# Optimization experiments

Measured on AMD Instinct MI355X. Metric: run time of the kernel, lower is better.

## Reference

```python
import jax, jax.numpy as jnp
import numpy as np

N = 100000   # nodes
E = 1600000  # edges
IN = 768     # in_dim
H = 128      # hidden_dim
G = 64       # graphs per batch


def setup_inputs() -> dict:
    key = jax.random.key(0)
    ks = jax.random.split(key, 9)
    x = jax.random.normal(ks[0], (N, IN), jnp.float32)
    edge_index = jax.random.randint(ks[1], (2, E), 0, N, dtype=jnp.int64)
    batch = jnp.sort(jax.random.randint(ks[2], (N,), 0, G, dtype=jnp.int64))
    W1 = jax.random.normal(ks[3], (IN, H), jnp.float32) / np.float32(np.sqrt(IN))
    b1 = jax.random.normal(ks[4], (H,), jnp.float32) * 0.01
    W2 = jax.random.normal(ks[5], (H, H), jnp.float32) / np.float32(np.sqrt(H))
    b2 = jax.random.normal(ks[6], (H,), jnp.float32) * 0.01
    Wh = jax.random.normal(ks[7], (H, 2), jnp.float32) / np.float32(np.sqrt(H))
    bh = jax.random.normal(ks[8], (2,), jnp.float32) * 0.01
    return dict(x=x, edge_index=edge_index, batch=batch, W1=W1, b1=b1,
                W2=W2, b2=b2, Wh=Wh, bh=bh, num_graphs=G)


def gcn_conv(x, src, dst, W, b, n):
    # PyG GCNConv default: add self-loops (already in src/dst), symmetric norm.
    deg = jax.ops.segment_sum(jnp.ones_like(dst, x.dtype), dst, num_segments=n)
    dis = jnp.where(deg > 0, jax.lax.rsqrt(deg), jnp.zeros_like(deg))
    h = x @ W                                   # [n, out]
    norm = (dis[src] * dis[dst])[:, None]       # [E+n, 1]
    out = jax.ops.segment_sum(h[src] * norm, dst, num_segments=n)
    return out + b


def reference(x, edge_index, batch, W1, b1, W2, b2, Wh, bh, num_graphs):
    n = x.shape[0]
    loop = jnp.arange(n, dtype=edge_index.dtype)
    src = jnp.concatenate([edge_index[0], loop])
    dst = jnp.concatenate([edge_index[1], loop])
    h = jax.nn.relu(gcn_conv(x, src, dst, W1, b1, n))   # dropout = eval identity
    h = jax.nn.relu(gcn_conv(h, src, dst, W2, b2, n))
    summed = jax.ops.segment_sum(h, batch, num_segments=num_graphs)
    counts = jax.ops.segment_sum(jnp.ones((n, 1), h.dtype), batch, num_segments=num_graphs)
    emb = summed / jnp.maximum(counts, 1.0)             # global_mean_pool
    return emb @ Wh + bh
```

## Files before the change

### kernel.cpp

```cpp
#include <hip/hip_runtime.h>
#include <hip/hip_bf16.h>
#include <hip/hip_fp16.h>

static constexpr int N_NODES  = 100000;
static constexpr int N_EDGES  = 1600000;
static constexpr int DIM_IN   = 768;
static constexpr int DIM_H    = 128;
static constexpr int N_GRAPHS = 64;
static constexpr int NB_SCAN  = (N_NODES + 255) / 256;

typedef __attribute__((ext_vector_type(8))) _Float16 half8;
typedef __attribute__((ext_vector_type(4))) float f32x4;

__global__ void k_convW(const float* __restrict__ W1, const float* __restrict__ W2,
                        _Float16* __restrict__ W1t, _Float16* __restrict__ W2t) {
    int i = blockIdx.x * 256 + threadIdx.x;
    const int total1 = DIM_IN * DIM_H;
    if (i < total1) {
        int k = i >> 7, n = i & 127;
        W1t[(size_t)n * DIM_IN + k] = (_Float16)W1[i];
    } else if (i < total1 + DIM_H * DIM_H) {
        int j = i - total1;
        int k = j >> 7, n = j & 127;
        W2t[(size_t)n * DIM_H + k] = (_Float16)W2[j];
    }
}

__global__ void k_scan1(const int* __restrict__ indeg, int* __restrict__ rp,
                        int* __restrict__ bsum, float* __restrict__ dis) {
    __shared__ int s[256];
    int t = threadIdx.x;
    int i = blockIdx.x * 256 + t;
    int v = (i < N_NODES) ? indeg[i] : 0;
    s[t] = v;
    __syncthreads();
    for (int off = 1; off < 256; off <<= 1) {
        int x = (t >= off) ? s[t - off] : 0;
        __syncthreads();
        s[t] += x;
        __syncthreads();
    }
    if (i < N_NODES) {
        rp[i] = s[t] - v;
        dis[i] = rsqrtf((float)v + 1.0f);
    }
    if (t == 255) bsum[blockIdx.x] = s[255];
}

__global__ void k_scan2(int* __restrict__ bsum, const int* __restrict__ batch,
                        int* __restrict__ gstart) {
    __shared__ int s[512];
    int t = threadIdx.x;
    int v = (t < NB_SCAN) ? bsum[t] : 0;
    s[t] = v;
    __syncthreads();
    for (int off = 1; off < 512; off <<= 1) {
        int x = (t >= off) ? s[t - off] : 0;
        __syncthreads();
        s[t] += x;
        __syncthreads();
    }
    if (t < NB_SCAN) bsum[t] = s[t] - v;
    if (t <= N_GRAPHS) {
        int lo = 0, hi = N_NODES;
        while (lo < hi) {
            int mid = (lo + hi) >> 1;
            if (batch[mid] < t) lo = mid + 1; else hi = mid;
        }
        gstart[t] = lo;
    }
}

__global__ void k_fixup(const int* __restrict__ rp, const int* __restrict__ bsum,
                        int* __restrict__ rpg, int* __restrict__ cursor2) {
    int i = blockIdx.x * 256 + threadIdx.x;
    if (i < N_NODES) {
        int v = rp[i] + bsum[i >> 8];
        rpg[i] = v;
        cursor2[i] = v;
    }
}

__global__ void k_scatter(const int* __restrict__ esrc, const int* __restrict__ edst,
                          const float* __restrict__ dis,
                          int* __restrict__ cursor2, uint2* __restrict__ csrw) {
    int e = blockIdx.x * 256 + threadIdx.x;
    if (e >= N_EDGES) return;
    int d = edst[e];
    int sv = esrc[e];
    int pos = atomicAdd(&cursor2[d], 1);
    uint2 val;
    val.x = (uint)sv;
    val.y = __float_as_uint(dis[sv]);
    csrw[pos] = val;
}

#define BKV 64
#define LDSTR 72

template<int K, bool AFP32, bool FUSE_INDEG>
__global__ __launch_bounds__(256) void k_gemm_mfma(const void* __restrict__ Av,
                                                   const _Float16* __restrict__ Wt,
                                                   _Float16* __restrict__ C,
                                                   int nrows,
                                                   const int* __restrict__ edst,
                                                   int* __restrict__ indeg,
                                                   int gemm_blocks) {
    __shared__ ushort As[64 * LDSTR];
    __shared__ ushort Bs[128 * LDSTR];

    if (FUSE_INDEG && (int)blockIdx.x >= gemm_blocks) {
        int e = (blockIdx.x - gemm_blocks) * 256 + threadIdx.x;
        if (e < N_EDGES) atomicAdd(&indeg[edst[e]], 1);
        return;
    }

    const int t = threadIdx.x;
    const int row0 = blockIdx.x * 64;
    const int sa_row = t >> 2;
    const int sa_col = (t & 3) * 16;
    const int sw_row = t >> 1;
    const int sw_col = (t & 1) * 32;
    const int l = t & 63;
    const int wv = t >> 6;
    const int wm = wv >> 1, wn = wv & 1;
    const int lr = l & 15;
    const int lk8 = (l >> 4) * 8;
    const bool arow_ok = (row0 + sa_row < nrows);

    f32x4 acc[2][4];
    const f32x4 zero = {0.f, 0.f, 0.f, 0.f};
    #pragma unroll
    for (int m = 0; m < 2; ++m)
        #pragma unroll
        for (int n = 0; n < 4; ++n) acc[m][n] = zero;

    for (int k0 = 0; k0 < K; k0 += BKV) {
        if (AFP32) {
            union { _Float16 h[16]; uint4 q[2]; } cv;
            float f[16];
            if (arow_ok) {
                const float4* Ap = (const float4*)((const float*)Av +
                    (size_t)(row0 + sa_row) * K + k0 + sa_col);
                #pragma unroll
                for (int i = 0; i < 4; ++i) *(float4*)&f[4 * i] = Ap[i];
            } else {
                #pragma unroll
                for (int i = 0; i < 16; ++i) f[i] = 0.f;
            }
            #pragma unroll
            for (int i = 0; i < 16; ++i) cv.h[i] = (_Float16)f[i];
            *(uint4*)&As[sa_row * LDSTR + sa_col]     = cv.q[0];
            *(uint4*)&As[sa_row * LDSTR + sa_col + 8] = cv.q[1];
        } else {
            uint4 q0 = {0, 0, 0, 0}, q1 = {0, 0, 0, 0};
            if (arow_ok) {
                const uint4* Ap = (const uint4*)((const _Float16*)Av +
                    (size_t)(row0 + sa_row) * K + k0 + sa_col);
                q0 = Ap[0]; q1 = Ap[1];
            }
            *(uint4*)&As[sa_row * LDSTR + sa_col]     = q0;
            *(uint4*)&As[sa_row * LDSTR + sa_col + 8] = q1;
        }
        {
            const uint4* Wp = (const uint4*)(Wt + (size_t)sw_row * K + k0 + sw_col);
            uint4 w0 = Wp[0], w1 = Wp[1], w2 = Wp[2], w3 = Wp[3];
            *(uint4*)&Bs[sw_row * LDSTR + sw_col + 0]  = w0;
            *(uint4*)&Bs[sw_row * LDSTR + sw_col + 8]  = w1;
            *(uint4*)&Bs[sw_row * LDSTR + sw_col + 16] = w2;
            *(uint4*)&Bs[sw_row * LDSTR + sw_col + 24] = w3;
        }
        __syncthreads();

        #pragma unroll
        for (int ks2 = 0; ks2 < 2; ++ks2) {
            half8 a[2], b[4];
            #pragma unroll
            for (int m = 0; m < 2; ++m)
                a[m] = *(const half8*)&As[(wm * 32 + m * 16 + lr) * LDSTR + ks2 * 32 + lk8];
            #pragma unroll
            for (int n = 0; n < 4; ++n)
                b[n] = *(const half8*)&Bs[(wn * 64 + n * 16 + lr) * LDSTR + ks2 * 32 + lk8];
            #pragma unroll
            for (int m = 0; m < 2; ++m)
                #pragma unroll
                for (int n = 0; n < 4; ++n)
                    acc[m][n] = __builtin_amdgcn_mfma_f32_16x16x32_f16(a[m], b[n], acc[m][n], 0, 0, 0);
        }
        __syncthreads();
    }

    #pragma unroll
    for (int m = 0; m < 2; ++m) {
        #pragma unroll
        for (int n = 0; n < 4; ++n) {
            int col = wn * 64 + n * 16 + lr;
            #pragma unroll
            for (int j = 0; j < 4; ++j) {
                int row = row0 + wm * 32 + m * 16 + (l >> 4) * 4 + j;
                if (row < nrows)
                    C[(size_t)row * DIM_H + col] = (_Float16)acc[m][n][j];
            }
        }
    }
}

__device__ __forceinline__ void acc8(uint4 u, float w, float* a) {
    __half2 h0 = *(__half2*)&u.x;
    __half2 h1 = *(__half2*)&u.y;
    __half2 h2 = *(__half2*)&u.z;
    __half2 h3 = *(__half2*)&u.w;
    a[0] += __low2float(h0) * w; a[1] += __high2float(h0) * w;
    a[2] += __low2float(h1) * w; a[3] += __high2float(h1) * w;
    a[4] += __low2float(h2) * w; a[5] += __high2float(h2) * w;
    a[6] += __low2float(h3) * w; a[7] += __high2float(h3) * w;
}

__global__ __launch_bounds__(256) void k_agg(const _Float16* __restrict__ hin,
                                             const uint2* __restrict__ csrw,
                                             const int* __restrict__ rpg,
                                             const int* __restrict__ indeg,
                                             const float* __restrict__ dis,
                                             const float* __restrict__ bias,
                                             _Float16* __restrict__ hout) {
    int node = (blockIdx.x * 256 + threadIdx.x) >> 6;
    int lane = threadIdx.x & 63;
    if (node >= N_NODES) return;
    int q  = lane >> 4;
    int cl = lane & 15;
    float di = dis[node];
    int beg = rpg[node];
    int cnt = indeg[node];

    float a[8] = {0.f, 0.f, 0.f, 0.f, 0.f, 0.f, 0.f, 0.f};

    {
        uint s; float w;
        if (q == 0)             { s = (uint)node; w = di * di; }
        else if (q - 1 < cnt)   { uint2 p = csrw[beg + q - 1]; s = p.x; w = __uint_as_float(p.y) * di; }
        else                    { s = (uint)node; w = 0.f; }
        uint4 u = ((const uint4*)(hin + (size_t)s * DIM_H))[cl];
        acc8(u, w, a);
    }
    const uint2* cp = csrw + beg + 3;
    int m = cnt - 3;
    int i = 0;
    for (; i + 8 <= m; i += 8) {
        uint2 p0 = cp[i + q];
        uint2 p1 = cp[i + 4 + q];
        float w0 = __uint_as_float(p0.y) * di;
        float w1 = __uint_as_float(p1.y) * di;
        uint4 u0 = ((const uint4*)(hin + (size_t)p0.x * DIM_H))[cl];
        uint4 u1 = ((const uint4*)(hin + (size_t)p1.x * DIM_H))[cl];
        acc8(u0, w0, a);
        acc8(u1, w1, a);
    }
    for (; i < m; i += 4) {
        int idx = i + q;
        uint s; float w;
        if (idx < m) { uint2 p = cp[idx]; s = p.x; w = __uint_as_float(p.y) * di; }
        else         { s = (uint)node;    w = 0.f; }
        uint4 u = ((const uint4*)(hin + (size_t)s * DIM_H))[cl];
        acc8(u, w, a);
    }

    #pragma unroll
    for (int j = 0; j < 8; ++j) {
        a[j] += __shfl_xor(a[j], 16);
        a[j] += __shfl_xor(a[j], 32);
    }

    if (q == 0) {
        float4 b0 = ((const float4*)bias)[cl * 2];
        float4 b1 = ((const float4*)bias)[cl * 2 + 1];
        __half2 h0 = __floats2half2_rn(fmaxf(a[0] + b0.x, 0.f), fmaxf(a[1] + b0.y, 0.f));
        __half2 h1 = __floats2half2_rn(fmaxf(a[2] + b0.z, 0.f), fmaxf(a[3] + b0.w, 0.f));
        __half2 h2 = __floats2half2_rn(fmaxf(a[4] + b1.x, 0.f), fmaxf(a[5] + b1.y, 0.f));
        __half2 h3 = __floats2half2_rn(fmaxf(a[6] + b1.z, 0.f), fmaxf(a[7] + b1.w, 0.f));
        uint4 o;
        o.x = *(uint*)&h0; o.y = *(uint*)&h1; o.z = *(uint*)&h2; o.w = *(uint*)&h3;
        ((uint4*)(hout + (size_t)node * DIM_H))[cl] = o;
    }
}

#define PSPLIT 8
__global__ __launch_bounds__(256) void k_pool(const _Float16* __restrict__ h,
                                              const int* __restrict__ gstart,
                                              float* __restrict__ pooled2) {
    int g  = blockIdx.x >> 3;
    int sp = blockIdx.x & 7;
    int r0 = gstart[g], r1 = gstart[g + 1];
    int count = r1 - r0;
    int chunk = (count + PSPLIT - 1) / PSPLIT;
    int aS = r0 + sp * chunk;
    int bE = min(aS + chunk, r1);
    int c  = threadIdx.x & 63;
    int rr = threadIdx.x >> 6;
    float s0a = 0.f, s1a = 0.f, s0b = 0.f, s1b = 0.f;
    int r = aS + rr;
    for (; r + 4 < bE; r += 8) {
        uint ua = ((const uint*)(h + (size_t)r * DIM_H))[c];
        uint ub = ((const uint*)(h + (size_t)(r + 4) * DIM_H))[c];
        __half2 ha = *(__half2*)&ua;
        __half2 hb = *(__half2*)&ub;
        s0a += __low2float(ha); s1a += __high2float(ha);
        s0b += __low2float(hb); s1b += __high2float(hb);
    }
    if (r < bE) {
        uint ua = ((const uint*)(h + (size_t)r * DIM_H))[c];
        __half2 ha = *(__half2*)&ua;
        s0a += __low2float(ha); s1a += __high2float(ha);
    }
    float s0 = s0a + s0b, s1 = s1a + s1b;
    __shared__ float sm0[4][64], sm1[4][64];
    sm0[rr][c] = s0; sm1[rr][c] = s1;
    __syncthreads();
    if (rr == 0) {
        float v0 = sm0[0][c] + sm0[1][c] + sm0[2][c] + sm0[3][c];
        float v1 = sm1[0][c] + sm1[1][c] + sm1[2][c] + sm1[3][c];
        float* dst = pooled2 + (size_t)(g * PSPLIT + sp) * DIM_H;
        dst[2 * c]     = v0;
        dst[2 * c + 1] = v1;
    }
}

__global__ __launch_bounds__(128) void k_head(const float* __restrict__ pooled2,
                                              const int* __restrict__ gstart,
                                              const float* __restrict__ Wh,
                                              const float* __restrict__ bh,
                                              float* __restrict__ out) {
    int g = blockIdx.x;
    int c = threadIdx.x;
    float s = 0.f;
    #pragma unroll
    for (int sp = 0; sp < PSPLIT; ++sp)
        s += pooled2[(size_t)(g * PSPLIT + sp) * DIM_H + c];
    float cntg = (float)(gstart[g + 1] - gstart[g]);
    float e = s / fmaxf(cntg, 1.0f);
    __shared__ float s0[128], s1[128];
    s0[c] = e * Wh[c * 2 + 0];
    s1[c] = e * Wh[c * 2 + 1];
    __syncthreads();
    for (int off = 64; off > 0; off >>= 1) {
        if (c < off) { s0[c] += s0[c + off]; s1[c] += s1[c + off]; }
        __syncthreads();
    }
    if (c == 0) {
        out[g * 2 + 0] = s0[0] + bh[0];
        out[g * 2 + 1] = s1[0] + bh[1];
    }
}

extern "C" void kernel_launch(void* const* d_in, const int* in_sizes, int n_in,
                              void* d_out, int out_size, void* d_ws, size_t ws_size,
                              hipStream_t stream) {
    const float* x    = (const float*)d_in[0];
    const int*   esrc = (const int*)d_in[1];
    const int*   edst = esrc + N_EDGES;
    const int*   batch= (const int*)d_in[2];
    const float* W1   = (const float*)d_in[3];
    const float* b1   = (const float*)d_in[4];
    const float* W2   = (const float*)d_in[5];
    const float* b2   = (const float*)d_in[6];
    const float* Wh   = (const float*)d_in[7];
    const float* bh   = (const float*)d_in[8];
    float* out = (float*)d_out;

    char* ws = (char*)d_ws;
    size_t off = 0;
    auto alloc = [&](size_t bytes) {
        void* p = ws + off;
        off += (bytes + 255) & ~(size_t)255;
        return p;
    };
    _Float16* bufZ   = (_Float16*)alloc((size_t)N_NODES * DIM_H * 2);
    _Float16* bufH   = (_Float16*)alloc((size_t)N_NODES * DIM_H * 2);
    float*    dis    = (float*)alloc((size_t)N_NODES * 4);
    int*      indeg  = (int*)  alloc((size_t)N_NODES * 4);
    int*      rp     = (int*)  alloc((size_t)N_NODES * 4);
    int*      rpg    = (int*)  alloc((size_t)N_NODES * 4);
    int*      cursor2= (int*)  alloc((size_t)N_NODES * 4);
    uint2*    csrw   = (uint2*)alloc((size_t)N_EDGES * 8);
    int*      bsum   = (int*)  alloc(512 * 4);
    float*    pooled2= (float*)alloc((size_t)N_GRAPHS * PSPLIT * DIM_H * 4);
    int*      gstart = (int*)  alloc((N_GRAPHS + 1) * 4);
    _Float16* W1t    = (_Float16*)alloc((size_t)DIM_IN * DIM_H * 2);
    _Float16* W2t    = (_Float16*)alloc((size_t)DIM_H * DIM_H * 2);

    hipMemsetAsync(indeg, 0, (size_t)N_NODES * 4, stream);

    int convblocks = (DIM_IN * DIM_H + DIM_H * DIM_H + 255) / 256;
    k_convW  <<<convblocks, 256, 0, stream>>>(W1, W2, W1t, W2t);

    int gblocks = (N_NODES + 63) / 64;
    int eblocks = (N_EDGES + 255) / 256;
    k_gemm_mfma<DIM_IN, true, true><<<gblocks + eblocks, 256, 0, stream>>>(
        x, W1t, bufZ, N_NODES, edst, indeg, gblocks);
    k_scan1  <<<NB_SCAN, 256, 0, stream>>>(indeg, rp, bsum, dis);
    k_scan2  <<<1, 512, 0, stream>>>(bsum, batch, gstart);
    k_fixup  <<<NB_SCAN, 256, 0, stream>>>(rp, bsum, rpg, cursor2);
    k_scatter<<<eblocks, 256, 0, stream>>>(esrc, edst, dis, cursor2, csrw);

    k_agg<<<(N_NODES + 3) / 4, 256, 0, stream>>>(bufZ, csrw, rpg, indeg, dis, b1, bufH);
    k_gemm_mfma<DIM_H, false, false><<<gblocks, 256, 0, stream>>>(
        bufH, W2t, bufZ, N_NODES, nullptr, nullptr, gblocks);
    k_agg<<<(N_NODES + 3) / 4, 256, 0, stream>>>(bufZ, csrw, rpg, indeg, dis, b2, bufH);

    k_pool<<<N_GRAPHS * PSPLIT, 256, 0, stream>>>(bufH, gstart, pooled2);
    k_head<<<N_GRAPHS, 128, 0, stream>>>(pooled2, gstart, Wh, bh, out);
}
```

Baseline: 386.6 us.

## Fold symmetric GCN normalization into row scaling and shrink CSR to source indices

Factors the per-edge weight dis[src]*dis[dst] out of aggregation. Source rows are pre-scaled by dis (the layer-1 features in a separate pass fused into the scatter launch, the layer-2 input by scaling the layer-1 aggregation output), and the destination factor is applied once per node. The CSR entry shrinks from 8 to 4 bytes, which halves edge-list traffic in both aggregations and drops the dis gather in the scatter. The cost is an extra read-modify-write pass over the layer-1 features and slightly different fp16 rounding.

New measurement: 425.0 us. +9.9%, slower.

```diff
diff --git a/kernel.cpp b/kernel.cpp
--- a/kernel.cpp
+++ b/kernel.cpp
@@ -81,18 +81,34 @@
     }
 }
 
-__global__ void k_scatter(const int* __restrict__ esrc, const int* __restrict__ edst,
-                          const float* __restrict__ dis,
-                          int* __restrict__ cursor2, uint2* __restrict__ csrw) {
-    int e = blockIdx.x * 256 + threadIdx.x;
-    if (e >= N_EDGES) return;
-    int d = edst[e];
-    int sv = esrc[e];
-    int pos = atomicAdd(&cursor2[d], 1);
-    uint2 val;
-    val.x = (uint)sv;
-    val.y = __float_as_uint(dis[sv]);
-    csrw[pos] = val;
+#define SCALE_U4 (N_NODES * DIM_H / 8)
+__global__ void k_scatscale(const int* __restrict__ esrc, const int* __restrict__ edst,
+                            int* __restrict__ cursor2, uint* __restrict__ csr,
+                            const float* __restrict__ dis, uint4* __restrict__ bufZ4,
+                            int scat_blocks) {
+    int b = blockIdx.x;
+    if (b < scat_blocks) {
+        int e = b * 256 + threadIdx.x;
+        if (e < N_EDGES) {
+            int d = edst[e];
+            int pos = atomicAdd(&cursor2[d], 1);
+            csr[pos] = (uint)esrc[e];
+        }
+        return;
+    }
+    int i = (b - scat_blocks) * 256 + threadIdx.x;
+    if (i >= SCALE_U4) return;
+    int row = i >> 4;
+    float d = dis[row];
+    uint4 u = bufZ4[i];
+    uint* w = (uint*)&u;
+    #pragma unroll
+    for (int j = 0; j < 4; ++j) {
+        __half2 h = *(__half2*)&w[j];
+        __half2 r = __floats2half2_rn(__low2float(h) * d, __high2float(h) * d);
+        w[j] = *(uint*)&r;
+    }
+    bufZ4[i] = u;
 }
 
 #define BKV 64
@@ -216,8 +232,9 @@
     a[6] += __low2float(h3) * w; a[7] += __high2float(h3) * w;
 }
 
+template<bool SCALE_OUT>
 __global__ __launch_bounds__(256) void k_agg(const _Float16* __restrict__ hin,
-                                             const uint2* __restrict__ csrw,
+                                             const uint* __restrict__ csr,
                                              const int* __restrict__ rpg,
                                              const int* __restrict__ indeg,
                                              const float* __restrict__ dis,
@@ -235,31 +252,29 @@
     float a[8] = {0.f, 0.f, 0.f, 0.f, 0.f, 0.f, 0.f, 0.f};
 
     {
-        uint s; float w;
-        if (q == 0)             { s = (uint)node; w = di * di; }
-        else if (q - 1 < cnt)   { uint2 p = csrw[beg + q - 1]; s = p.x; w = __uint_as_float(p.y) * di; }
+        uint s; float w = 1.f;
+        if (q == 0)             { s = (uint)node; }
+        else if (q - 1 < cnt)   { s = csr[beg + q - 1]; }
         else                    { s = (uint)node; w = 0.f; }
         uint4 u = ((const uint4*)(hin + (size_t)s * DIM_H))[cl];
         acc8(u, w, a);
     }
-    const uint2* cp = csrw + beg + 3;
+    const uint* cp = csr + beg + 3;
     int m = cnt - 3;
     int i = 0;
     for (; i + 8 <= m; i += 8) {
-        uint2 p0 = cp[i + q];
-        uint2 p1 = cp[i + 4 + q];
-        float w0 = __uint_as_float(p0.y) * di;
-        float w1 = __uint_as_float(p1.y) * di;
-        uint4 u0 = ((const uint4*)(hin + (size_t)p0.x * DIM_H))[cl];
-        uint4 u1 = ((const uint4*)(hin + (size_t)p1.x * DIM_H))[cl];
-        acc8(u0, w0, a);
-        acc8(u1, w1, a);
+        uint s0 = cp[i + q];
+        uint s1 = cp[i + 4 + q];
+        uint4 u0 = ((const uint4*)(hin + (size_t)s0 * DIM_H))[cl];
+        uint4 u1 = ((const uint4*)(hin + (size_t)s1 * DIM_H))[cl];
+        acc8(u0, 1.f, a);
+        acc8(u1, 1.f, a);
     }
     for (; i < m; i += 4) {
         int idx = i + q;
-        uint s; float w;
-        if (idx < m) { uint2 p = cp[idx]; s = p.x; w = __uint_as_float(p.y) * di; }
-        else         { s = (uint)node;    w = 0.f; }
+        uint s; float w = 1.f;
+        if (idx < m) { s = cp[idx]; }
+        else         { s = (uint)node; w = 0.f; }
         uint4 u = ((const uint4*)(hin + (size_t)s * DIM_H))[cl];
         acc8(u, w, a);
     }
@@ -273,13 +288,20 @@
     if (q == 0) {
         float4 b0 = ((const float4*)bias)[cl * 2];
         float4 b1 = ((const float4*)bias)[cl * 2 + 1];
-        __half2 h0 = __floats2half2_rn(fmaxf(a[0] + b0.x, 0.f), fmaxf(a[1] + b0.y, 0.f));
-        __half2 h1 = __floats2half2_rn(fmaxf(a[2] + b0.z, 0.f), fmaxf(a[3] + b0.w, 0.f));
-        __half2 h2 = __floats2half2_rn(fmaxf(a[4] + b1.x, 0.f), fmaxf(a[5] + b1.y, 0.f));
-        __half2 h3 = __floats2half2_rn(fmaxf(a[6] + b1.z, 0.f), fmaxf(a[7] + b1.w, 0.f));
-        uint4 o;
-        o.x = *(uint*)&h0; o.y = *(uint*)&h1; o.z = *(uint*)&h2; o.w = *(uint*)&h3;
-        ((uint4*)(hout + (size_t)node * DIM_H))[cl] = o;
+        float bb[8] = {b0.x, b0.y, b0.z, b0.w, b1.x, b1.y, b1.z, b1.w};
+        float o[8];
+        #pragma unroll
+        for (int j = 0; j < 8; ++j) {
+            float v = fmaxf(di * a[j] + bb[j], 0.f);
+            o[j] = SCALE_OUT ? v * di : v;
+        }
+        __half2 h0 = __floats2half2_rn(o[0], o[1]);
+        __half2 h1 = __floats2half2_rn(o[2], o[3]);
+        __half2 h2 = __floats2half2_rn(o[4], o[5]);
+        __half2 h3 = __floats2half2_rn(o[6], o[7]);
+        uint4 ov;
+        ov.x = *(uint*)&h0; ov.y = *(uint*)&h1; ov.z = *(uint*)&h2; ov.w = *(uint*)&h3;
+        ((uint4*)(hout + (size_t)node * DIM_H))[cl] = ov;
     }
 }
 
@@ -380,7 +402,7 @@
     int*      rp     = (int*)  alloc((size_t)N_NODES * 4);
     int*      rpg    = (int*)  alloc((size_t)N_NODES * 4);
     int*      cursor2= (int*)  alloc((size_t)N_NODES * 4);
-    uint2*    csrw   = (uint2*)alloc((size_t)N_EDGES * 8);
+    uint*     csr    = (uint*) alloc((size_t)N_EDGES * 4);
     int*      bsum   = (int*)  alloc(512 * 4);
     float*    pooled2= (float*)alloc((size_t)N_GRAPHS * PSPLIT * DIM_H * 4);
     int*      gstart = (int*)  alloc((N_GRAPHS + 1) * 4);
@@ -394,17 +416,19 @@
 
     int gblocks = (N_NODES + 63) / 64;
     int eblocks = (N_EDGES + 255) / 256;
+    int zblocks = (SCALE_U4 + 255) / 256;
     k_gemm_mfma<DIM_IN, true, true><<<gblocks + eblocks, 256, 0, stream>>>(
         x, W1t, bufZ, N_NODES, edst, indeg, gblocks);
     k_scan1  <<<NB_SCAN, 256, 0, stream>>>(indeg, rp, bsum, dis);
     k_scan2  <<<1, 512, 0, stream>>>(bsum, batch, gstart);
     k_fixup  <<<NB_SCAN, 256, 0, stream>>>(rp, bsum, rpg, cursor2);
-    k_scatter<<<eblocks, 256, 0, stream>>>(esrc, edst, dis, cursor2, csrw);
-
-    k_agg<<<(N_NODES + 3) / 4, 256, 0, stream>>>(bufZ, csrw, rpg, indeg, dis, b1, bufH);
+    k_scatscale<<<eblocks + zblocks, 256, 0, stream>>>(esrc, edst, cursor2, csr,
+                                                       dis, (uint4*)bufZ, eblocks);
+
+    k_agg<true ><<<(N_NODES + 3) / 4, 256, 0, stream>>>(bufZ, csr, rpg, indeg, dis, b1, bufH);
     k_gemm_mfma<DIM_H, false, false><<<gblocks, 256, 0, stream>>>(
         bufH, W2t, bufZ, N_NODES, nullptr, nullptr, gblocks);
-    k_agg<<<(N_NODES + 3) / 4, 256, 0, stream>>>(bufZ, csrw, rpg, indeg, dis, b2, bufH);
+    k_agg<false><<<(N_NODES + 3) / 4, 256, 0, stream>>>(bufZ, csr, rpg, indeg, dis, b2, bufH);
 
     k_pool<<<N_GRAPHS * PSPLIT, 256, 0, stream>>>(bufH, gstart, pooled2);
     k_head<<<N_GRAPHS, 128, 0, stream>>>(pooled2, gstart, Wh, bh, out);
```
